# Kernel tuning notes

Measured on AMD Instinct MI355X. Metric: run time of the kernel, lower is better.

Reference implementation:

```python
import jax, jax.numpy as jnp
import numpy as np

EMBED = 128
HEADS = 32
HEAD_DIM = EMBED // HEADS  # 4
BATCH = 32
SEQ = 2048


def setup_inputs() -> dict:
    key = jax.random.key(0)
    ks = jax.random.split(key, 6)
    s = 1.0 / np.sqrt(EMBED)
    return {
        "x": jax.random.normal(ks[0], (BATCH, SEQ, EMBED), dtype=jnp.float32),
        # torch Linear weights are (out_features, in_features)
        "Wq": jax.random.uniform(ks[1], (EMBED, EMBED), jnp.float32, -s, s),
        "Wk": jax.random.uniform(ks[2], (EMBED, EMBED), jnp.float32, -s, s),
        "Wv": jax.random.uniform(ks[3], (EMBED, EMBED), jnp.float32, -s, s),
        "Wo": jax.random.uniform(ks[4], (EMBED, EMBED), jnp.float32, -s, s),
        "bo": jax.random.uniform(ks[5], (EMBED,), jnp.float32, -s, s),
    }


def reference(x, Wq, Wk, Wv, Wo, bo):
    b, s, e = x.shape
    h, d = HEADS, HEAD_DIM
    # projections (torch Linear: x @ W.T)
    q = (x @ Wq.T).reshape(b, s, h, d)
    k = (x @ Wk.T).reshape(b, s, h, d)
    v = (x @ Wv.T).reshape(b, s, h, d)
    # FAITHFUL to source: einsum 'bnqh,bnkh->bnqk' on (b, seq, heads, head_dim)
    # => n = seq position, q/k = HEADS. Attention is over the heads axis.
    scale = 1.0 / (float(d) ** 0.5)
    scores = jnp.einsum('bnqh,bnkh->bnqk', q, k) * scale  # (b, seq, heads, heads)
    attn = jax.nn.softmax(scores, axis=-1)
    attended = jnp.einsum('bnqk,bnkv->bnqv', attn, v).reshape(b, s, e)
    return attended @ Wo.T + bo
```

## Files before the change

### kernel.cpp

```cpp
#include <hip/hip_runtime.h>


#define TOKENS (32 * 2048)
#define E 128
#define NH 32
#define WTOK 16
#define THREADS 128
#define LPITCH 136

typedef __attribute__((ext_vector_type(4))) float f32x4;
typedef __attribute__((ext_vector_type(16))) float f32x16;
typedef __fp16 h8_t __attribute__((ext_vector_type(8)));

#if __has_builtin(__builtin_amdgcn_exp2f)
#define EXP2F __builtin_amdgcn_exp2f
#else
#define EXP2F exp2f
#endif

#if __has_builtin(__builtin_amdgcn_rcpf)
#define RCPF __builtin_amdgcn_rcpf
#else
#define RCPF(x) (1.0f / (x))
#endif

static __device__ __forceinline__ unsigned pk16(float a, float b) {
    return __builtin_bit_cast(unsigned, __builtin_amdgcn_cvt_pkrtz(a, b));
}

static __device__ __forceinline__ f32x16 zero16() {
    f32x16 z;
#pragma unroll
    for (int i = 0; i < 16; ++i) z[i] = 0.f;
    return z;
}

static __device__ __forceinline__ int vperm(int kh) {
    return ((kh >> 4) & 1) * 16 + ((kh >> 2) & 1) * 8 + ((kh >> 3) & 1) * 4 + (kh & 3);
}

__global__ void pack_w(const float* __restrict__ Wq, const float* __restrict__ Wk,
                       const float* __restrict__ Wv, const float* __restrict__ Wo,
                       __fp16* __restrict__ wpk) {
    int idx = blockIdx.x * blockDim.x + threadIdx.x;
    if (idx >= 4 * 8 * 4 * 64) return;
    int lane = idx & 63;
    int ks   = (idx >> 6) & 3;
    int nt   = (idx >> 8) & 7;
    int proj = idx >> 11;
    const float* W = (proj == 0) ? Wq : (proj == 1) ? Wk : (proj == 2) ? Wv : Wo;
    float scl = (proj == 1) ? 0.72134752044448170f : 1.0f;
    int c = lane & 15, g = lane >> 4;
    const float* src = W + (size_t)(nt * 16 + c) * E + ks * 32 + g * 8;
    __fp16* dst = wpk + (size_t)idx * 8;
#pragma unroll
    for (int j = 0; j < 8; ++j) dst[j] = (__fp16)(src[j] * scl);
}

__global__ __launch_bounds__(THREADS) void mha_fused(
        const float* __restrict__ x, const __fp16* __restrict__ wpk,
        const float* __restrict__ bo, float* __restrict__ out) {
    __shared__ __align__(16) __fp16 qs [2 * WTOK * LPITCH];
    __shared__ __align__(16) __fp16 ksh[2 * WTOK * LPITCH];
    __shared__ __align__(16) __fp16 vth[2 * WTOK * LPITCH];

    const int tid  = threadIdx.x;
    const int wave = tid >> 6;
    const int lane = tid & 63;
    const int c = lane & 15, g = lane >> 4;
    const int tbase = blockIdx.x * (2 * WTOK) + wave * WTOK;

    __fp16* qsw = qs  + wave * WTOK * LPITCH;
    __fp16* ksw = ksh + wave * WTOK * LPITCH;
    __fp16* vtw = vth + wave * WTOK * LPITCH;

    {
        h8_t afrag[4];
        const float* xrow = x + (size_t)(tbase + c) * E;
#pragma unroll
        for (int ks2 = 0; ks2 < 4; ++ks2) {
            const float* p = xrow + ks2 * 32 + g * 8;
            float4 v0 = *(const float4*)(p);
            float4 v1 = *(const float4*)(p + 4);
            uint4 au;
            au.x = pk16(v0.x, v0.y);
            au.y = pk16(v0.z, v0.w);
            au.z = pk16(v1.x, v1.y);
            au.w = pk16(v1.z, v1.w);
            afrag[ks2] = __builtin_bit_cast(h8_t, au);
        }

#pragma unroll
        for (int nc = 0; nc < 24; ++nc) {
            int proj = nc >> 3;
            int nt   = nc & 7;
            const __fp16* wb = wpk + ((size_t)((proj * 8 + nt) * 4) * 64 + lane) * 8;
            f32x4 acc = {0.f, 0.f, 0.f, 0.f};
#pragma unroll
            for (int ks2 = 0; ks2 < 4; ++ks2) {
                h8_t wf = *(const h8_t*)(wb + (size_t)ks2 * 64 * 8);
                acc = __builtin_amdgcn_mfma_f32_16x16x32_f16(wf, afrag[ks2], acc, 0, 0, 0);
            }
            if (proj < 2) {
                __fp16* dst = proj ? ksw : qsw;
                uint2 st = make_uint2(pk16(acc[0], acc[1]), pk16(acc[2], acc[3]));
                *(uint2*)(dst + c * LPITCH + nt * 16 + g * 4) = st;
            } else {
                int vp = vperm(nt * 4 + g);
#pragma unroll
                for (int r2 = 0; r2 < 4; ++r2)
                    vtw[c * LPITCH + r2 * 32 + vp] = (__fp16)acc[r2];
            }
        }
    }

    {
        const int c32 = lane & 31;
        const int gg  = lane >> 5;
        const uint4 ONES4 = make_uint4(0x3C003C00u, 0x3C003C00u, 0x3C003C00u, 0x3C003C00u);
        const f32x16 z = zero16();
#pragma unroll 1
        for (int pr = 0; pr < 8; ++pr) {
            const int t0 = pr * 2, t1 = t0 + 1;
            const __fp16* v0r = vtw + t0 * LPITCH;
            const __fp16* v1r = vtw + t1 * LPITCH;

            uint4 ka0 = {0u,0u,0u,0u}, qa0 = {0u,0u,0u,0u};
            uint4 ka1 = {0u,0u,0u,0u}, qa1 = {0u,0u,0u,0u};
            if (gg == 0) {
                uint2 t;
                t = *(const uint2*)(ksw + t0 * LPITCH + c32 * 4); ka0.x = t.x; ka0.y = t.y;
                t = *(const uint2*)(qsw + t0 * LPITCH + c32 * 4); qa0.x = t.x; qa0.y = t.y;
                t = *(const uint2*)(ksw + t1 * LPITCH + c32 * 4); ka1.x = t.x; ka1.y = t.y;
                t = *(const uint2*)(qsw + t1 * LPITCH + c32 * 4); qa1.x = t.x; qa1.y = t.y;
            }
            uint4 va00 = *(const uint4*)(v0r + (c32 & 3) * 32 + gg * 8);
            uint4 va01 = *(const uint4*)(v0r + (c32 & 3) * 32 + 16 + gg * 8);
            uint4 va10 = *(const uint4*)(v1r + (c32 & 3) * 32 + gg * 8);
            uint4 va11 = *(const uint4*)(v1r + (c32 & 3) * 32 + 16 + gg * 8);
            if (c32 == 4) { va00 = ONES4; va01 = ONES4; va10 = ONES4; va11 = ONES4; }

            f32x16 sc0 = __builtin_amdgcn_mfma_f32_32x32x16_f16(
                __builtin_bit_cast(h8_t, ka0), __builtin_bit_cast(h8_t, qa0), z, 0, 0, 0);
            f32x16 sc1 = __builtin_amdgcn_mfma_f32_32x32x16_f16(
                __builtin_bit_cast(h8_t, ka1), __builtin_bit_cast(h8_t, qa1), z, 0, 0, 0);

            uint4 p00u, p01u, p10u, p11u;
            {
                float e[16];
#pragma unroll
                for (int r = 0; r < 16; ++r) e[r] = EXP2F(sc0[r]);
                p00u = make_uint4(pk16(e[0], e[1]),  pk16(e[2], e[3]),
                                  pk16(e[4], e[5]),  pk16(e[6], e[7]));
                p01u = make_uint4(pk16(e[8], e[9]),  pk16(e[10], e[11]),
                                  pk16(e[12], e[13]), pk16(e[14], e[15]));
            }
            {
                float e[16];
#pragma unroll
                for (int r = 0; r < 16; ++r) e[r] = EXP2F(sc1[r]);
                p10u = make_uint4(pk16(e[0], e[1]),  pk16(e[2], e[3]),
                                  pk16(e[4], e[5]),  pk16(e[6], e[7]));
                p11u = make_uint4(pk16(e[8], e[9]),  pk16(e[10], e[11]),
                                  pk16(e[12], e[13]), pk16(e[14], e[15]));
            }

            f32x16 pv0 = __builtin_amdgcn_mfma_f32_32x32x16_f16(
                __builtin_bit_cast(h8_t, va00), __builtin_bit_cast(h8_t, p00u), z, 0, 0, 0);
            pv0 = __builtin_amdgcn_mfma_f32_32x32x16_f16(
                __builtin_bit_cast(h8_t, va01), __builtin_bit_cast(h8_t, p01u), pv0, 0, 0, 0);
            f32x16 pv1 = __builtin_amdgcn_mfma_f32_32x32x16_f16(
                __builtin_bit_cast(h8_t, va10), __builtin_bit_cast(h8_t, p10u), z, 0, 0, 0);
            pv1 = __builtin_amdgcn_mfma_f32_32x32x16_f16(
                __builtin_bit_cast(h8_t, va11), __builtin_bit_cast(h8_t, p11u), pv1, 0, 0, 0);

            float s0 = __shfl(pv0[0], c32 + 32, 64);
            float s1 = __shfl(pv1[0], c32 + 32, 64);
            float r0 = RCPF(s0), r1 = RCPF(s1);
            if (lane < 32) {
                uint2 st0 = make_uint2(pk16(pv0[0] * r0, pv0[1] * r0),
                                       pk16(pv0[2] * r0, pv0[3] * r0));
                uint2 st1 = make_uint2(pk16(pv1[0] * r1, pv1[1] * r1),
                                       pk16(pv1[2] * r1, pv1[3] * r1));
                *(uint2*)(qsw + t0 * LPITCH + c32 * 4) = st0;
                *(uint2*)(qsw + t1 * LPITCH + c32 * 4) = st1;
            }
        }
    }

    {
        h8_t af[4];
#pragma unroll
        for (int ks2 = 0; ks2 < 4; ++ks2)
            af[ks2] = *(const h8_t*)(qsw + c * LPITCH + ks2 * 32 + g * 8);
#pragma unroll
        for (int nt = 0; nt < 8; ++nt) {
            const __fp16* wb = wpk + ((size_t)((3 * 8 + nt) * 4) * 64 + lane) * 8;
            f32x4 acc = {0.f, 0.f, 0.f, 0.f};
#pragma unroll
            for (int ks2 = 0; ks2 < 4; ++ks2) {
                h8_t b = *(const h8_t*)(wb + (size_t)ks2 * 64 * 8);
                acc = __builtin_amdgcn_mfma_f32_16x16x32_f16(b, af[ks2], acc, 0, 0, 0);
            }
            int col0 = nt * 16 + g * 4;
            float4 b4 = *(const float4*)(bo + col0);
            float4 st = make_float4(acc[0] + b4.x, acc[1] + b4.y,
                                    acc[2] + b4.z, acc[3] + b4.w);
            *(float4*)(out + (size_t)(tbase + c) * E + col0) = st;
        }
    }
}

extern "C" void kernel_launch(void* const* d_in, const int* in_sizes, int n_in,
                              void* d_out, int out_size, void* d_ws, size_t ws_size,
                              hipStream_t stream) {
    const float* x  = (const float*)d_in[0];
    const float* Wq = (const float*)d_in[1];
    const float* Wk = (const float*)d_in[2];
    const float* Wv = (const float*)d_in[3];
    const float* Wo = (const float*)d_in[4];
    const float* bo = (const float*)d_in[5];
    __fp16* wpk = (__fp16*)d_ws;
    float* out = (float*)d_out;

    pack_w<<<32, 256, 0, stream>>>(Wq, Wk, Wv, Wo, wpk);
    mha_fused<<<TOKENS / (2 * WTOK), THREADS, 0, stream>>>(x, wpk, bo, out);
}
```

Before: 42.17 us.

## Software-pipeline weight fragment loads and LDS operand loads across MFMA stages

Adds a 3-deep register ring of prefetched packed-weight fragments in the QKV projection and output projection loops, so global/L2 weight loads for tile n+3 are issued while MFMAs for tile n run. The per-token attention loop is fully unrolled and double-buffers its LDS loads of K, Q and V for the next token pair. The goal is to hide load latency behind MFMA and exp work. The cost is much higher VGPR pressure, 48 extra h8 registers for the weight ring, which may reduce occupancy or cause spills.

Result: no change. 41.53 us (-1.5%).

```diff
diff --git a/kernel.cpp b/kernel.cpp
--- a/kernel.cpp
+++ b/kernel.cpp
@@ -90,16 +90,30 @@
             afrag[ks2] = __builtin_bit_cast(h8_t, au);
         }
 
+        h8_t wfb[3][4];
+#pragma unroll
+        for (int p = 0; p < 3; ++p) {
+            const __fp16* wb = wpk + ((size_t)(p * 4) * 64 + lane) * 8;
+#pragma unroll
+            for (int k = 0; k < 4; ++k)
+                wfb[p][k] = *(const h8_t*)(wb + (size_t)k * 64 * 8);
+        }
+
 #pragma unroll
         for (int nc = 0; nc < 24; ++nc) {
-            int proj = nc >> 3;
-            int nt   = nc & 7;
-            const __fp16* wb = wpk + ((size_t)((proj * 8 + nt) * 4) * 64 + lane) * 8;
+            const int proj = nc >> 3;
+            const int nt   = nc & 7;
+            const int slot = nc % 3;
             f32x4 acc = {0.f, 0.f, 0.f, 0.f};
 #pragma unroll
             for (int ks2 = 0; ks2 < 4; ++ks2) {
-                h8_t wf = *(const h8_t*)(wb + (size_t)ks2 * 64 * 8);
-                acc = __builtin_amdgcn_mfma_f32_16x16x32_f16(wf, afrag[ks2], acc, 0, 0, 0);
+                acc = __builtin_amdgcn_mfma_f32_16x16x32_f16(wfb[slot][ks2], afrag[ks2], acc, 0, 0, 0);
+            }
+            if (nc + 3 < 24) {
+                const __fp16* wb = wpk + ((size_t)((nc + 3) * 4) * 64 + lane) * 8;
+#pragma unroll
+                for (int k = 0; k < 4; ++k)
+                    wfb[slot][k] = *(const h8_t*)(wb + (size_t)k * 64 * 8);
             }
             if (proj < 2) {
                 __fp16* dst = proj ? ksw : qsw;
@@ -119,31 +133,39 @@
         const int gg  = lane >> 5;
         const uint4 ONES4 = make_uint4(0x3C003C00u, 0x3C003C00u, 0x3C003C00u, 0x3C003C00u);
         const f32x16 z = zero16();
-#pragma unroll 1
+
+        uint4 ka0[2], qa0[2], ka1[2], qa1[2];
+        uint4 va00[2], va01[2], va10[2], va11[2];
+
+#define LOADPAIR(s, pr_) do {                                                  \
+        const int t0_ = (pr_) * 2, t1_ = t0_ + 1;                              \
+        ka0[s] = qa0[s] = ka1[s] = qa1[s] = make_uint4(0u, 0u, 0u, 0u);        \
+        if (gg == 0) {                                                         \
+            uint2 t_;                                                          \
+            t_ = *(const uint2*)(ksw + t0_ * LPITCH + c32 * 4); ka0[s].x = t_.x; ka0[s].y = t_.y; \
+            t_ = *(const uint2*)(qsw + t0_ * LPITCH + c32 * 4); qa0[s].x = t_.x; qa0[s].y = t_.y; \
+            t_ = *(const uint2*)(ksw + t1_ * LPITCH + c32 * 4); ka1[s].x = t_.x; ka1[s].y = t_.y; \
+            t_ = *(const uint2*)(qsw + t1_ * LPITCH + c32 * 4); qa1[s].x = t_.x; qa1[s].y = t_.y; \
+        }                                                                      \
+        va00[s] = *(const uint4*)(vtw + t0_ * LPITCH + (c32 & 3) * 32 + gg * 8);      \
+        va01[s] = *(const uint4*)(vtw + t0_ * LPITCH + (c32 & 3) * 32 + 16 + gg * 8); \
+        va10[s] = *(const uint4*)(vtw + t1_ * LPITCH + (c32 & 3) * 32 + gg * 8);      \
+        va11[s] = *(const uint4*)(vtw + t1_ * LPITCH + (c32 & 3) * 32 + 16 + gg * 8); \
+        if (c32 == 4) { va00[s] = ONES4; va01[s] = ONES4; va10[s] = ONES4; va11[s] = ONES4; } \
+    } while (0)
+
+        LOADPAIR(0, 0);
+#pragma unroll
         for (int pr = 0; pr < 8; ++pr) {
+            const int s = pr & 1;
+            if (pr < 7) LOADPAIR(s ^ 1, pr + 1);
+
             const int t0 = pr * 2, t1 = t0 + 1;
-            const __fp16* v0r = vtw + t0 * LPITCH;
-            const __fp16* v1r = vtw + t1 * LPITCH;
-
-            uint4 ka0 = {0u,0u,0u,0u}, qa0 = {0u,0u,0u,0u};
-            uint4 ka1 = {0u,0u,0u,0u}, qa1 = {0u,0u,0u,0u};
-            if (gg == 0) {
-                uint2 t;
-                t = *(const uint2*)(ksw + t0 * LPITCH + c32 * 4); ka0.x = t.x; ka0.y = t.y;
-                t = *(const uint2*)(qsw + t0 * LPITCH + c32 * 4); qa0.x = t.x; qa0.y = t.y;
-                t = *(const uint2*)(ksw + t1 * LPITCH + c32 * 4); ka1.x = t.x; ka1.y = t.y;
-                t = *(const uint2*)(qsw + t1 * LPITCH + c32 * 4); qa1.x = t.x; qa1.y = t.y;
-            }
-            uint4 va00 = *(const uint4*)(v0r + (c32 & 3) * 32 + gg * 8);
-            uint4 va01 = *(const uint4*)(v0r + (c32 & 3) * 32 + 16 + gg * 8);
-            uint4 va10 = *(const uint4*)(v1r + (c32 & 3) * 32 + gg * 8);
-            uint4 va11 = *(const uint4*)(v1r + (c32 & 3) * 32 + 16 + gg * 8);
-            if (c32 == 4) { va00 = ONES4; va01 = ONES4; va10 = ONES4; va11 = ONES4; }
 
             f32x16 sc0 = __builtin_amdgcn_mfma_f32_32x32x16_f16(
-                __builtin_bit_cast(h8_t, ka0), __builtin_bit_cast(h8_t, qa0), z, 0, 0, 0);
+                __builtin_bit_cast(h8_t, ka0[s]), __builtin_bit_cast(h8_t, qa0[s]), z, 0, 0, 0);
             f32x16 sc1 = __builtin_amdgcn_mfma_f32_32x32x16_f16(
-                __builtin_bit_cast(h8_t, ka1), __builtin_bit_cast(h8_t, qa1), z, 0, 0, 0);
+                __builtin_bit_cast(h8_t, ka1[s]), __builtin_bit_cast(h8_t, qa1[s]), z, 0, 0, 0);
 
             uint4 p00u, p01u, p10u, p11u;
             {
@@ -166,13 +188,13 @@
             }
 
             f32x16 pv0 = __builtin_amdgcn_mfma_f32_32x32x16_f16(
-                __builtin_bit_cast(h8_t, va00), __builtin_bit_cast(h8_t, p00u), z, 0, 0, 0);
+                __builtin_bit_cast(h8_t, va00[s]), __builtin_bit_cast(h8_t, p00u), z, 0, 0, 0);
             pv0 = __builtin_amdgcn_mfma_f32_32x32x16_f16(
-                __builtin_bit_cast(h8_t, va01), __builtin_bit_cast(h8_t, p01u), pv0, 0, 0, 0);
+                __builtin_bit_cast(h8_t, va01[s]), __builtin_bit_cast(h8_t, p01u), pv0, 0, 0, 0);
             f32x16 pv1 = __builtin_amdgcn_mfma_f32_32x32x16_f16(
-                __builtin_bit_cast(h8_t, va10), __builtin_bit_cast(h8_t, p10u), z, 0, 0, 0);
+                __builtin_bit_cast(h8_t, va10[s]), __builtin_bit_cast(h8_t, p10u), z, 0, 0, 0);
             pv1 = __builtin_amdgcn_mfma_f32_32x32x16_f16(
-                __builtin_bit_cast(h8_t, va11), __builtin_bit_cast(h8_t, p11u), pv1, 0, 0, 0);
+                __builtin_bit_cast(h8_t, va11[s]), __builtin_bit_cast(h8_t, p11u), pv1, 0, 0, 0);
 
             float s0 = __shfl(pv0[0], c32 + 32, 64);
             float s1 = __shfl(pv1[0], c32 + 32, 64);
@@ -186,6 +208,7 @@
                 *(uint2*)(qsw + t1 * LPITCH + c32 * 4) = st1;
             }
         }
+#undef LOADPAIR
     }
 
     {
@@ -193,14 +216,28 @@
 #pragma unroll
         for (int ks2 = 0; ks2 < 4; ++ks2)
             af[ks2] = *(const h8_t*)(qsw + c * LPITCH + ks2 * 32 + g * 8);
+
+        h8_t wob[3][4];
+#pragma unroll
+        for (int p = 0; p < 3; ++p) {
+            const __fp16* wb = wpk + ((size_t)((3 * 8 + p) * 4) * 64 + lane) * 8;
+#pragma unroll
+            for (int k = 0; k < 4; ++k)
+                wob[p][k] = *(const h8_t*)(wb + (size_t)k * 64 * 8);
+        }
+
 #pragma unroll
         for (int nt = 0; nt < 8; ++nt) {
-            const __fp16* wb = wpk + ((size_t)((3 * 8 + nt) * 4) * 64 + lane) * 8;
+            const int slot = nt % 3;
             f32x4 acc = {0.f, 0.f, 0.f, 0.f};
 #pragma unroll
-            for (int ks2 = 0; ks2 < 4; ++ks2) {
-                h8_t b = *(const h8_t*)(wb + (size_t)ks2 * 64 * 8);
-                acc = __builtin_amdgcn_mfma_f32_16x16x32_f16(b, af[ks2], acc, 0, 0, 0);
+            for (int ks2 = 0; ks2 < 4; ++ks2)
+                acc = __builtin_amdgcn_mfma_f32_16x16x32_f16(wob[slot][ks2], af[ks2], acc, 0, 0, 0);
+            if (nt + 3 < 8) {
+                const __fp16* wb = wpk + ((size_t)((3 * 8 + nt + 3) * 4) * 64 + lane) * 8;
+#pragma unroll
+                for (int k = 0; k < 4; ++k)
+                    wob[slot][k] = *(const h8_t*)(wb + (size_t)k * 64 * 8);
             }
             int col0 = nt * 16 + g * 4;
             float4 b4 = *(const float4*)(bo + col0);
```

## Use single-wave blocks and stop unrolling projection loops to cut register pressure

Applied to the files above, without the earlier changes.

Each block now holds one wave of 16 tokens instead of two waves, which doubles the grid and halves shared memory per block. The projection and output GEMM loops switch from full unroll to unroll 1, loading the four weight fragments explicitly per iteration. The Q/K and V projections are split into separate loops so the per-iteration branch goes away. The aim is lower VGPR usage and finer-grained scheduling for higher occupancy, at the cost of less instruction-level parallelism and less overlap of weight loads with MFMA.

Result: slower. 53.42 us (+26.7%).

```diff
diff --git a/kernel.cpp b/kernel.cpp
--- a/kernel.cpp
+++ b/kernel.cpp
@@ -5,7 +5,7 @@
 #define E 128
 #define NH 32
 #define WTOK 16
-#define THREADS 128
+#define THREADS 64
 #define LPITCH 136
 
 typedef __attribute__((ext_vector_type(4))) float f32x4;
@@ -60,19 +60,13 @@
 __global__ __launch_bounds__(THREADS) void mha_fused(
         const float* __restrict__ x, const __fp16* __restrict__ wpk,
         const float* __restrict__ bo, float* __restrict__ out) {
-    __shared__ __align__(16) __fp16 qs [2 * WTOK * LPITCH];
-    __shared__ __align__(16) __fp16 ksh[2 * WTOK * LPITCH];
-    __shared__ __align__(16) __fp16 vth[2 * WTOK * LPITCH];
-
-    const int tid  = threadIdx.x;
-    const int wave = tid >> 6;
-    const int lane = tid & 63;
+    __shared__ __align__(16) __fp16 qsw[WTOK * LPITCH];
+    __shared__ __align__(16) __fp16 ksw[WTOK * LPITCH];
+    __shared__ __align__(16) __fp16 vtw[WTOK * LPITCH];
+
+    const int lane = threadIdx.x & 63;
     const int c = lane & 15, g = lane >> 4;
-    const int tbase = blockIdx.x * (2 * WTOK) + wave * WTOK;
-
-    __fp16* qsw = qs  + wave * WTOK * LPITCH;
-    __fp16* ksw = ksh + wave * WTOK * LPITCH;
-    __fp16* vtw = vth + wave * WTOK * LPITCH;
+    const int tbase = blockIdx.x * WTOK;
 
     {
         h8_t afrag[4];
@@ -90,27 +84,40 @@
             afrag[ks2] = __builtin_bit_cast(h8_t, au);
         }
 
-#pragma unroll
-        for (int nc = 0; nc < 24; ++nc) {
-            int proj = nc >> 3;
-            int nt   = nc & 7;
-            const __fp16* wb = wpk + ((size_t)((proj * 8 + nt) * 4) * 64 + lane) * 8;
-            f32x4 acc = {0.f, 0.f, 0.f, 0.f};
-#pragma unroll
-            for (int ks2 = 0; ks2 < 4; ++ks2) {
-                h8_t wf = *(const h8_t*)(wb + (size_t)ks2 * 64 * 8);
-                acc = __builtin_amdgcn_mfma_f32_16x16x32_f16(wf, afrag[ks2], acc, 0, 0, 0);
-            }
-            if (proj < 2) {
-                __fp16* dst = proj ? ksw : qsw;
-                uint2 st = make_uint2(pk16(acc[0], acc[1]), pk16(acc[2], acc[3]));
-                *(uint2*)(dst + c * LPITCH + nt * 16 + g * 4) = st;
-            } else {
-                int vp = vperm(nt * 4 + g);
-#pragma unroll
-                for (int r2 = 0; r2 < 4; ++r2)
-                    vtw[c * LPITCH + r2 * 32 + vp] = (__fp16)acc[r2];
-            }
+        const f32x4 z4 = {0.f, 0.f, 0.f, 0.f};
+
+#pragma unroll 1
+        for (int nc = 0; nc < 16; ++nc) {
+            const __fp16* wb = wpk + ((size_t)(nc * 4) * 64 + lane) * 8;
+            h8_t w0 = *(const h8_t*)(wb);
+            h8_t w1 = *(const h8_t*)(wb + 512);
+            h8_t w2 = *(const h8_t*)(wb + 1024);
+            h8_t w3 = *(const h8_t*)(wb + 1536);
+            f32x4 acc = __builtin_amdgcn_mfma_f32_16x16x32_f16(w0, afrag[0], z4, 0, 0, 0);
+            acc = __builtin_amdgcn_mfma_f32_16x16x32_f16(w1, afrag[1], acc, 0, 0, 0);
+            acc = __builtin_amdgcn_mfma_f32_16x16x32_f16(w2, afrag[2], acc, 0, 0, 0);
+            acc = __builtin_amdgcn_mfma_f32_16x16x32_f16(w3, afrag[3], acc, 0, 0, 0);
+            __fp16* dst = (nc < 8) ? qsw : ksw;
+            int nt = nc & 7;
+            uint2 st = make_uint2(pk16(acc[0], acc[1]), pk16(acc[2], acc[3]));
+            *(uint2*)(dst + c * LPITCH + nt * 16 + g * 4) = st;
+        }
+#pragma unroll 1
+        for (int nc = 16; nc < 24; ++nc) {
+            const __fp16* wb = wpk + ((size_t)(nc * 4) * 64 + lane) * 8;
+            h8_t w0 = *(const h8_t*)(wb);
+            h8_t w1 = *(const h8_t*)(wb + 512);
+            h8_t w2 = *(const h8_t*)(wb + 1024);
+            h8_t w3 = *(const h8_t*)(wb + 1536);
+            f32x4 acc = __builtin_amdgcn_mfma_f32_16x16x32_f16(w0, afrag[0], z4, 0, 0, 0);
+            acc = __builtin_amdgcn_mfma_f32_16x16x32_f16(w1, afrag[1], acc, 0, 0, 0);
+            acc = __builtin_amdgcn_mfma_f32_16x16x32_f16(w2, afrag[2], acc, 0, 0, 0);
+            acc = __builtin_amdgcn_mfma_f32_16x16x32_f16(w3, afrag[3], acc, 0, 0, 0);
+            int nt = nc & 7;
+            int vp = vperm(nt * 4 + g);
+#pragma unroll
+            for (int r2 = 0; r2 < 4; ++r2)
+                vtw[c * LPITCH + r2 * 32 + vp] = (__fp16)acc[r2];
         }
     }
 
@@ -119,11 +126,10 @@
         const int gg  = lane >> 5;
         const uint4 ONES4 = make_uint4(0x3C003C00u, 0x3C003C00u, 0x3C003C00u, 0x3C003C00u);
         const f32x16 z = zero16();
+
 #pragma unroll 1
         for (int pr = 0; pr < 8; ++pr) {
             const int t0 = pr * 2, t1 = t0 + 1;
-            const __fp16* v0r = vtw + t0 * LPITCH;
-            const __fp16* v1r = vtw + t1 * LPITCH;
 
             uint4 ka0 = {0u,0u,0u,0u}, qa0 = {0u,0u,0u,0u};
             uint4 ka1 = {0u,0u,0u,0u}, qa1 = {0u,0u,0u,0u};
@@ -134,10 +140,10 @@
                 t = *(const uint2*)(ksw + t1 * LPITCH + c32 * 4); ka1.x = t.x; ka1.y = t.y;
                 t = *(const uint2*)(qsw + t1 * LPITCH + c32 * 4); qa1.x = t.x; qa1.y = t.y;
             }
-            uint4 va00 = *(const uint4*)(v0r + (c32 & 3) * 32 + gg * 8);
-            uint4 va01 = *(const uint4*)(v0r + (c32 & 3) * 32 + 16 + gg * 8);
-            uint4 va10 = *(const uint4*)(v1r + (c32 & 3) * 32 + gg * 8);
-            uint4 va11 = *(const uint4*)(v1r + (c32 & 3) * 32 + 16 + gg * 8);
+            uint4 va00 = *(const uint4*)(vtw + t0 * LPITCH + (c32 & 3) * 32 + gg * 8);
+            uint4 va01 = *(const uint4*)(vtw + t0 * LPITCH + (c32 & 3) * 32 + 16 + gg * 8);
+            uint4 va10 = *(const uint4*)(vtw + t1 * LPITCH + (c32 & 3) * 32 + gg * 8);
+            uint4 va11 = *(const uint4*)(vtw + t1 * LPITCH + (c32 & 3) * 32 + 16 + gg * 8);
             if (c32 == 4) { va00 = ONES4; va01 = ONES4; va10 = ONES4; va11 = ONES4; }
 
             f32x16 sc0 = __builtin_amdgcn_mfma_f32_32x32x16_f16(
@@ -193,15 +199,19 @@
 #pragma unroll
         for (int ks2 = 0; ks2 < 4; ++ks2)
             af[ks2] = *(const h8_t*)(qsw + c * LPITCH + ks2 * 32 + g * 8);
-#pragma unroll
+
+        const f32x4 z4 = {0.f, 0.f, 0.f, 0.f};
+#pragma unroll 1
         for (int nt = 0; nt < 8; ++nt) {
-            const __fp16* wb = wpk + ((size_t)((3 * 8 + nt) * 4) * 64 + lane) * 8;
-            f32x4 acc = {0.f, 0.f, 0.f, 0.f};
-#pragma unroll
-            for (int ks2 = 0; ks2 < 4; ++ks2) {
-                h8_t b = *(const h8_t*)(wb + (size_t)ks2 * 64 * 8);
-                acc = __builtin_amdgcn_mfma_f32_16x16x32_f16(b, af[ks2], acc, 0, 0, 0);
-            }
+            const __fp16* wb = wpk + ((size_t)((24 + nt) * 4) * 64 + lane) * 8;
+            h8_t w0 = *(const h8_t*)(wb);
+            h8_t w1 = *(const h8_t*)(wb + 512);
+            h8_t w2 = *(const h8_t*)(wb + 1024);
+            h8_t w3 = *(const h8_t*)(wb + 1536);
+            f32x4 acc = __builtin_amdgcn_mfma_f32_16x16x32_f16(w0, af[0], z4, 0, 0, 0);
+            acc = __builtin_amdgcn_mfma_f32_16x16x32_f16(w1, af[1], acc, 0, 0, 0);
+            acc = __builtin_amdgcn_mfma_f32_16x16x32_f16(w2, af[2], acc, 0, 0, 0);
+            acc = __builtin_amdgcn_mfma_f32_16x16x32_f16(w3, af[3], acc, 0, 0, 0);
             int col0 = nt * 16 + g * 4;
             float4 b4 = *(const float4*)(bo + col0);
             float4 st = make_float4(acc[0] + b4.x, acc[1] + b4.y,
@@ -224,5 +234,5 @@
     float* out = (float*)d_out;
 
     pack_w<<<32, 256, 0, stream>>>(Wq, Wk, Wv, Wo, wpk);
-    mha_fused<<<TOKENS / (2 * WTOK), THREADS, 0, stream>>>(x, wpk, bo, out);
-}
+    mha_fused<<<TOKENS / WTOK, THREADS, 0, stream>>>(x, wpk, bo, out);
+}
```
